# Kernel tuning notes

Measured on AMD Instinct MI355X. Metric: run time of the kernel, lower is better.

The kernel has to match this reference:

```python
import jax, jax.numpy as jnp
import numpy as np
from jax import lax

K = 16  # number of KNN neighbors (fixed in module)


def _knn_neighbors(x, k):
    # x: (B, 3, N) point coordinates -> neighbor coords (B, 3, N, K)
    inner = jnp.einsum('bdn,bdm->bnm', x, x)          # (B, N, N)
    sq = jnp.sum(x * x, axis=1)                        # (B, N)
    d2 = sq[:, :, None] + sq[:, None, :] - 2.0 * inner  # pairwise sq dists (B, N, N)
    _, nbr_idx = lax.top_k(-d2, k)                     # k nearest (incl. self), (B, N, K)
    # gather neighbor coordinates: expand x to (B, 3, 1, N), idx to (B, 1, N, K)
    neighbor = jnp.take_along_axis(x[:, :, None, :], nbr_idx[:, None, :, :], axis=3)
    return neighbor  # (B, 3, N, K)


def _down_index(neighbor, x, npts_ds):
    # center-diff saliency: sum of squared offsets to K neighbors per point
    diff = neighbor - x[:, :, :, None]                 # (B, 3, N, K)
    score = jnp.sum(diff * diff, axis=(1, 3))          # (B, N)
    _, idx = lax.top_k(score, npts_ds)                 # (B, npts_ds)
    return idx


def setup_inputs() -> dict:
    key = jax.random.key(0)
    k1, k2 = jax.random.split(key)
    B, N, C = 8, 4096, 128
    x = jax.random.normal(k1, (B, 3, N), dtype=jnp.float32)
    y = jax.random.normal(k2, (B, C, N), dtype=jnp.float32)
    return {"x": x, "y": y, "npts_ds": 2048}


def reference(x, y, npts_ds):
    B, _, N = x.shape
    C = y.shape[1]
    neighbor = _knn_neighbors(x, K)                    # ops.group(x, K, 'neighbor')
    idx = _down_index(neighbor, x, npts_ds)            # ops.down_index(...), (B, npts_ds)
    idx3 = jnp.broadcast_to(idx[:, None, :], (B, 3, npts_ds))
    idxC = jnp.broadcast_to(idx[:, None, :], (B, C, npts_ds))
    top_k_xyz = jnp.take_along_axis(x, idx3, axis=2)    # (B, 3, npts_ds)
    top_k_points = jnp.take_along_axis(y, idxC, axis=2)  # (B, C, npts_ds)
    return (top_k_xyz, top_k_points)
```

## Files before the change

### kernel.cpp

```cpp
#include <hip/hip_runtime.h>
#include <math.h>

#define BATCH 8
#define NPTS 4096
#define CHAN 128
#define KNN 16
#define SPLIT 4
#define CHUNK (NPTS / SPLIT)
#define ISPLIT 2
#define QCH (CHUNK / ISPLIT)
#define PCAP 24
#define RSPLIT 4
#define RCHUNK (NPTS / RSPLIT)

typedef unsigned long long u64;

__device__ __forceinline__ u64 pack_key(float d2, int idx) {
  unsigned b = __float_as_uint(d2);
  b ^= (unsigned)((int)b >> 31) | 0x80000000u;
  return ((u64)b << 32) | (unsigned)idx;
}

__device__ __forceinline__ float d2_ref(float4 q, float ppx, float ppy,
                                        float ppz, float psq) {
  float inner = __fadd_rn(__fadd_rn(__fmul_rn(ppx, q.x), __fmul_rn(ppy, q.y)),
                          __fmul_rn(ppz, q.z));
  return __fsub_rn(__fadd_rn(psq, q.w), __fmul_rn(2.0f, inner));
}

__device__ __forceinline__ void ce_asc(u64& x, u64& y) {
  bool sw = y < x;
  u64 lo = sw ? y : x;
  u64 hi = sw ? x : y;
  x = lo;
  y = hi;
}

__device__ __forceinline__ void bitonic_sort32(u64 a[32]) {
#pragma unroll
  for (int k = 2; k <= 32; k <<= 1) {
#pragma unroll
    for (int j = k >> 1; j > 0; j >>= 1) {
#pragma unroll
      for (int i = 0; i < 32; ++i) {
        int l = i ^ j;
        if (l > i) {
          if ((i & k) == 0) ce_asc(a[i], a[l]);
          else              ce_asc(a[l], a[i]);
        }
      }
    }
  }
}

__device__ __forceinline__ void merge_keep16(u64 T[16], const u64 A[16]) {
  u64 nt[16];
#pragma unroll
  for (int i = 0; i < 16; ++i) {
    u64 a = A[15 - i];
    nt[i] = (a < T[i]) ? a : T[i];
  }
#pragma unroll
  for (int j = 8; j > 0; j >>= 1) {
#pragma unroll
    for (int i = 0; i < 16; ++i) {
      int l = i ^ j;
      if (l > i) ce_asc(nt[i], nt[l]);
    }
  }
#pragma unroll
  for (int i = 0; i < 16; ++i) T[i] = nt[i];
}

__device__ __forceinline__ void ce_i32(int& x, int& y) {
  int lo = (x < y) ? x : y;
  int hi = (x < y) ? y : x;
  x = lo;
  y = hi;
}

__device__ __forceinline__ void batcher_sort16_i32(int a[16]) {
#define CE(i, j) ce_i32(a[i], a[j])
  CE(0, 8); CE(1, 9); CE(2, 10); CE(3, 11);
  CE(4, 12); CE(5, 13); CE(6, 14); CE(7, 15);
  CE(0, 4); CE(1, 5); CE(2, 6); CE(3, 7);
  CE(8, 12); CE(9, 13); CE(10, 14); CE(11, 15);
  CE(4, 8); CE(5, 9); CE(6, 10); CE(7, 11);
  CE(0, 2); CE(1, 3); CE(4, 6); CE(5, 7);
  CE(8, 10); CE(9, 11); CE(12, 14); CE(13, 15);
  CE(2, 8); CE(3, 9); CE(6, 12); CE(7, 13);
  CE(2, 4); CE(3, 5); CE(6, 8); CE(7, 9); CE(10, 12); CE(11, 13);
  CE(0, 1); CE(2, 3); CE(4, 5); CE(6, 7);
  CE(8, 9); CE(10, 11); CE(12, 13); CE(14, 15);
  CE(1, 8); CE(3, 10); CE(5, 12); CE(7, 14);
  CE(1, 4); CE(3, 6); CE(5, 8); CE(7, 10); CE(9, 12); CE(11, 14);
  CE(1, 2); CE(3, 4); CE(5, 6); CE(7, 8); CE(9, 10); CE(11, 12); CE(13, 14);
#undef CE
}

__device__ __forceinline__ void merge_keep16_i32(int T[16], const int A[16]) {
  int nt[16];
#pragma unroll
  for (int i = 0; i < 16; ++i) {
    int a = A[15 - i];
    nt[i] = (a < T[i]) ? a : T[i];
  }
#pragma unroll
  for (int j = 8; j > 0; j >>= 1) {
#pragma unroll
    for (int i = 0; i < 16; ++i) {
      int l = i ^ j;
      if (l > i) ce_i32(nt[i], nt[l]);
    }
  }
#pragma unroll
  for (int i = 0; i < 16; ++i) T[i] = nt[i];
}

__global__ __attribute__((amdgpu_waves_per_eu(4, 4)))
__launch_bounds__(512) void knn_partial_kernel(
    const float* __restrict__ x, u64* __restrict__ pkey) {
  const int s = blockIdx.x % SPLIT;
  const int ntile = (blockIdx.x / SPLIT) % (NPTS / 256);
  const int b = blockIdx.x / (SPLIT * (NPTS / 256));
  const int p = threadIdx.x & 255;
  const int h = threadIdx.x >> 8;
  __shared__ float4 xs[CHUNK];
  __shared__ unsigned short idxbuf[512 * PCAP];
  __shared__ u64 mbuf[KNN][256];

  const float* xb = x + (size_t)b * 3 * NPTS;
  for (int i = threadIdx.x; i < CHUNK; i += 512) {
    int gm = s * CHUNK + i;
    float px = xb[gm];
    float py = xb[NPTS + gm];
    float pz = xb[2 * NPTS + gm];
    float sq = __fadd_rn(__fadd_rn(__fmul_rn(px, px), __fmul_rn(py, py)),
                         __fmul_rn(pz, pz));
    xs[i] = make_float4(px, py, pz, sq);
  }

  const int n = ntile * 256 + p;
  float ppx = xb[n];
  float ppy = xb[NPTS + n];
  float ppz = xb[2 * NPTS + n];
  float psq = __fadd_rn(__fadd_rn(__fmul_rn(ppx, ppx), __fmul_rn(ppy, ppy)),
                        __fmul_rn(ppz, ppz));
  __syncthreads();

  const int cbase = h * QCH;

  int T[16];
#pragma unroll
  for (int i = 0; i < 16; ++i) T[i] = 0x7FFFFFFF;

  for (int base = 0; base < QCH; base += 16) {
    int A[16];
#pragma unroll
    for (int t = 0; t < 16; ++t) {
      float4 q = xs[cbase + base + t];
      A[t] = __float_as_int(d2_ref(q, ppx, ppy, ppz, psq));
    }
    batcher_sort16_i32(A);
    merge_keep16_i32(T, A);
  }
  const int v15 = T[15];

  unsigned short* mybuf = &idxbuf[(unsigned)threadIdx.x * PCAP];
  int cnt = 0;
#pragma unroll 4
  for (int m = 0; m < QCH; ++m) {
    float4 q = xs[cbase + m];
    int bits = __float_as_int(d2_ref(q, ppx, ppy, ppz, psq));
    if (bits <= v15) {
      mybuf[cnt < PCAP - 1 ? cnt : PCAP - 1] = (unsigned short)(cbase + m);
      ++cnt;
    }
  }

  u64 K[32];
#pragma unroll
  for (int j = 0; j < PCAP; ++j) {
    int loc = mybuf[j] & (CHUNK - 1);
    float4 q = xs[loc];
    float d2 = d2_ref(q, ppx, ppy, ppz, psq);
    u64 k = pack_key(d2, s * CHUNK + loc);
    K[j] = (j < cnt) ? k : ~0ull;
  }
#pragma unroll
  for (int j = PCAP; j < 32; ++j) K[j] = ~0ull;
  bitonic_sort32(K);

  if (h == 1) {
#pragma unroll
    for (int j = 0; j < 16; ++j) mbuf[j][p] = K[j];
  }
  __syncthreads();
  if (h == 0) {
    u64 T64[16];
#pragma unroll
    for (int j = 0; j < 16; ++j) T64[j] = K[j];
    u64 A64[16];
#pragma unroll
    for (int j = 0; j < 16; ++j) A64[j] = mbuf[j][p];
    merge_keep16(T64, A64);
    u64* pb = pkey + ((size_t)(b * SPLIT + s) * KNN) * NPTS + n;
#pragma unroll
    for (int j = 0; j < 16; ++j) pb[(size_t)j * NPTS] = T64[j];
  }
}

__global__ __attribute__((amdgpu_waves_per_eu(1, 2)))
__launch_bounds__(256) void merge_score_kernel(
    const float* __restrict__ x, const u64* __restrict__ pkey,
    float* __restrict__ score, int* __restrict__ cnt) {
  const int b = blockIdx.x / (NPTS / 256);
  const int n = (blockIdx.x % (NPTS / 256)) * 256 + threadIdx.x;

  cnt[(size_t)b * NPTS + n] = 0;

  u64 T[16];
  {
    const u64* pb = pkey + ((size_t)(b * SPLIT + 0) * KNN) * NPTS + n;
#pragma unroll
    for (int j = 0; j < 16; ++j) T[j] = pb[(size_t)j * NPTS];
  }
#pragma unroll
  for (int s = 1; s < SPLIT; ++s) {
    const u64* pb = pkey + ((size_t)(b * SPLIT + s) * KNN) * NPTS + n;
    u64 A[16];
#pragma unroll
    for (int j = 0; j < 16; ++j) A[j] = pb[(size_t)j * NPTS];
    merge_keep16(T, A);
  }

  const float* xb = x + (size_t)b * 3 * NPTS;
  float ppx = xb[n];
  float ppy = xb[NPTS + n];
  float ppz = xb[2 * NPTS + n];

  float nx[KNN], ny[KNN], nz[KNN];
#pragma unroll
  for (int j = 0; j < KNN; ++j) {
    int idx = (int)(unsigned)T[j];
    nx[j] = xb[idx];
    ny[j] = xb[NPTS + idx];
    nz[j] = xb[2 * NPTS + idx];
  }

  float P[3];
#pragma unroll
  for (int d = 0; d < 3; ++d) {
    const float pc = (d == 0) ? ppx : ((d == 1) ? ppy : ppz);
    float r[8];
#pragma unroll
    for (int j = 0; j < 8; ++j) {
      float c0 = (d == 0) ? nx[j] : ((d == 1) ? ny[j] : nz[j]);
      float c1 = (d == 0) ? nx[j + 8] : ((d == 1) ? ny[j + 8] : nz[j + 8]);
      float e0 = __fsub_rn(c0, pc);
      float e1 = __fsub_rn(c1, pc);
      r[j] = __fadd_rn(__fmul_rn(e0, e0), __fmul_rn(e1, e1));
    }
    float t0 = __fadd_rn(r[0], r[1]);
    float t1 = __fadd_rn(r[2], r[3]);
    float t2 = __fadd_rn(r[4], r[5]);
    float t3 = __fadd_rn(r[6], r[7]);
    P[d] = __fadd_rn(__fadd_rn(t0, t1), __fadd_rn(t2, t3));
  }
  score[(size_t)b * NPTS + n] =
      __fadd_rn(__fadd_rn(P[0], P[1]), P[2]);
}

__global__ __launch_bounds__(256) void rank_partial_kernel(
    const float* __restrict__ score, int* __restrict__ cnt) {
  const int s = blockIdx.x % RSPLIT;
  const int ntile = (blockIdx.x / RSPLIT) % (NPTS / 256);
  const int b = blockIdx.x / (RSPLIT * (NPTS / 256));
  __shared__ float ss[RCHUNK];

  const float* sb = score + (size_t)b * NPTS;
  for (int i = threadIdx.x; i < RCHUNK; i += 256)
    ss[i] = sb[s * RCHUNK + i];

  const int n = ntile * 256 + threadIdx.x;
  const float sn = sb[n];
  __syncthreads();

  int c = 0;
#pragma unroll 8
  for (int mm = 0; mm < RCHUNK; ++mm) {
    float sm = ss[mm];
    int gm = s * RCHUNK + mm;
    c += (sm > sn) || (sm == sn && gm < n);
  }
  atomicAdd(&cnt[(size_t)b * NPTS + n], c);
}

__global__ __launch_bounds__(256) void rank_scatter_kernel(
    const int* __restrict__ cnt, int* __restrict__ sel, int npts) {
  int t = blockIdx.x * 256 + threadIdx.x;
  int b = t / NPTS;
  int n = t % NPTS;
  int c = cnt[t];
  if (c < npts) sel[(size_t)b * npts + c] = n;
}

__global__ __launch_bounds__(256) void gather_kernel(
    const float* __restrict__ x, const float* __restrict__ y,
    const int* __restrict__ sel, float* __restrict__ out, int npts,
    int total0, int total) {
  int tid = blockIdx.x * blockDim.x + threadIdx.x;
  if (tid >= total) return;
  if (tid < total0) {
    int j = tid % npts;
    int rest = tid / npts;
    int d = rest % 3;
    int b = rest / 3;
    int src = sel[b * npts + j];
    out[tid] = x[((size_t)b * 3 + d) * NPTS + src];
  } else {
    int t = tid - total0;
    int j = t % npts;
    int rest = t / npts;
    int c = rest % CHAN;
    int b = rest / CHAN;
    int src = sel[b * npts + j];
    out[tid] = y[((size_t)b * CHAN + c) * NPTS + src];
  }
}

extern "C" void kernel_launch(void* const* d_in, const int* in_sizes, int n_in,
                              void* d_out, int out_size, void* d_ws,
                              size_t ws_size, hipStream_t stream) {
  const float* x = (const float*)d_in[0];
  const float* y = (const float*)d_in[1];
  float* out = (float*)d_out;

  const int npts = out_size / (BATCH * (3 + CHAN));

  char* w = (char*)d_ws;
  u64* pkey = (u64*)w;
  w += sizeof(u64) * (size_t)BATCH * SPLIT * KNN * NPTS;
  float* score = (float*)w;
  w += sizeof(float) * (size_t)BATCH * NPTS;
  int* cnt = (int*)w;
  w += sizeof(int) * (size_t)BATCH * NPTS;
  int* sel = (int*)w;

  knn_partial_kernel<<<BATCH * (NPTS / 256) * SPLIT, 512, 0, stream>>>(
      x, pkey);
  merge_score_kernel<<<BATCH * NPTS / 256, 256, 0, stream>>>(x, pkey, score,
                                                             cnt);
  rank_partial_kernel<<<BATCH * (NPTS / 256) * RSPLIT, 256, 0, stream>>>(
      score, cnt);
  rank_scatter_kernel<<<BATCH * NPTS / 256, 256, 0, stream>>>(cnt, sel, npts);

  const int total0 = BATCH * 3 * npts;
  gather_kernel<<<(out_size + 255) / 256, 256, 0, stream>>>(
      x, y, sel, out, npts, total0, out_size);
}
```

Measured before the change: 268.3 us.

## Embed candidate index in truncated distance bits to skip rescan pass

Packs the local candidate index into the low 9 mantissa bits of each int-cast distance, so the running top-16 carries indices directly. A 17th-smallest tracker detects ties at the truncated threshold. Only in that case does it fall back to the full rescan-and-collect pass. The common path instead recomputes exact distances for the 16 kept candidates and sorts them with a 16-element network, removing a full second sweep over the chunk and the 32-element bitonic sort. The cost is extra min/max work per batch to maintain the 17th value, plus thread divergence when some lanes take the slow path.

```diff
diff --git a/kernel.cpp b/kernel.cpp
--- a/kernel.cpp
+++ b/kernel.cpp
@@ -9,7 +9,7 @@
 #define CHUNK (NPTS / SPLIT)
 #define ISPLIT 2
 #define QCH (CHUNK / ISPLIT)
-#define PCAP 24
+#define EPC 24
 #define RSPLIT 4
 #define RCHUNK (NPTS / RSPLIT)
 
@@ -34,6 +34,25 @@
   u64 hi = sw ? x : y;
   x = lo;
   y = hi;
+}
+
+__device__ __forceinline__ void batcher_sort16_u64(u64 a[16]) {
+#define CE(i, j) ce_asc(a[i], a[j])
+  CE(0, 8); CE(1, 9); CE(2, 10); CE(3, 11);
+  CE(4, 12); CE(5, 13); CE(6, 14); CE(7, 15);
+  CE(0, 4); CE(1, 5); CE(2, 6); CE(3, 7);
+  CE(8, 12); CE(9, 13); CE(10, 14); CE(11, 15);
+  CE(4, 8); CE(5, 9); CE(6, 10); CE(7, 11);
+  CE(0, 2); CE(1, 3); CE(4, 6); CE(5, 7);
+  CE(8, 10); CE(9, 11); CE(12, 14); CE(13, 15);
+  CE(2, 8); CE(3, 9); CE(6, 12); CE(7, 13);
+  CE(2, 4); CE(3, 5); CE(6, 8); CE(7, 9); CE(10, 12); CE(11, 13);
+  CE(0, 1); CE(2, 3); CE(4, 5); CE(6, 7);
+  CE(8, 9); CE(10, 11); CE(12, 13); CE(14, 15);
+  CE(1, 8); CE(3, 10); CE(5, 12); CE(7, 14);
+  CE(1, 4); CE(3, 6); CE(5, 8); CE(7, 10); CE(9, 12); CE(11, 14);
+  CE(1, 2); CE(3, 4); CE(5, 6); CE(7, 8); CE(9, 10); CE(11, 12); CE(13, 14);
+#undef CE
 }
 
 __device__ __forceinline__ void bitonic_sort32(u64 a[32]) {
@@ -126,7 +145,7 @@
   const int p = threadIdx.x & 255;
   const int h = threadIdx.x >> 8;
   __shared__ float4 xs[CHUNK];
-  __shared__ unsigned short idxbuf[512 * PCAP];
+  __shared__ unsigned short ebuf[512 * EPC];
   __shared__ u64 mbuf[KNN][256];
 
   const float* xb = x + (size_t)b * 3 * NPTS;
@@ -153,43 +172,75 @@
   int T[16];
 #pragma unroll
   for (int i = 0; i < 16; ++i) T[i] = 0x7FFFFFFF;
-
+  int r17 = 0x7FFFFFFF;
+
+#pragma unroll 1
   for (int base = 0; base < QCH; base += 16) {
     int A[16];
 #pragma unroll
     for (int t = 0; t < 16; ++t) {
       float4 q = xs[cbase + base + t];
-      A[t] = __float_as_int(d2_ref(q, ppx, ppy, ppz, psq));
+      int bits = __float_as_int(d2_ref(q, ppx, ppy, ppz, psq));
+      A[t] = (bits & 0xFFFFFE00) | (base + t);
     }
     batcher_sort16_i32(A);
+    int u[16];
+#pragma unroll
+    for (int i = 0; i < 16; ++i) {
+      int a = A[15 - i];
+      u[i] = (T[i] < a) ? a : T[i];
+    }
+#pragma unroll
+    for (int w = 8; w > 0; w >>= 1) {
+#pragma unroll
+      for (int i = 0; i < 16; ++i) {
+        if (i < w) u[i] = (u[i] < u[i + w]) ? u[i] : u[i + w];
+      }
+    }
+    r17 = (r17 < u[0]) ? r17 : u[0];
     merge_keep16_i32(T, A);
   }
-  const int v15 = T[15];
-
-  unsigned short* mybuf = &idxbuf[(unsigned)threadIdx.x * PCAP];
-  int cnt = 0;
+
+  const int tau = T[15] & 0xFFFFFE00;
+  const bool slow = ((r17 & 0xFFFFFE00) == tau);
+
+  u64 K[16];
+  if (!slow) {
+#pragma unroll
+    for (int j = 0; j < 16; ++j) {
+      int loc = cbase + (T[j] & 511);
+      float4 q = xs[loc];
+      float d2 = d2_ref(q, ppx, ppy, ppz, psq);
+      K[j] = pack_key(d2, s * CHUNK + loc);
+    }
+    batcher_sort16_u64(K);
+  } else {
+    unsigned short* myb = &ebuf[(unsigned)threadIdx.x * EPC];
+    int cnt = 0;
 #pragma unroll 4
-  for (int m = 0; m < QCH; ++m) {
-    float4 q = xs[cbase + m];
-    int bits = __float_as_int(d2_ref(q, ppx, ppy, ppz, psq));
-    if (bits <= v15) {
-      mybuf[cnt < PCAP - 1 ? cnt : PCAP - 1] = (unsigned short)(cbase + m);
-      ++cnt;
-    }
-  }
-
-  u64 K[32];
-#pragma unroll
-  for (int j = 0; j < PCAP; ++j) {
-    int loc = mybuf[j] & (CHUNK - 1);
-    float4 q = xs[loc];
-    float d2 = d2_ref(q, ppx, ppy, ppz, psq);
-    u64 k = pack_key(d2, s * CHUNK + loc);
-    K[j] = (j < cnt) ? k : ~0ull;
-  }
-#pragma unroll
-  for (int j = PCAP; j < 32; ++j) K[j] = ~0ull;
-  bitonic_sort32(K);
+    for (int m = 0; m < QCH; ++m) {
+      float4 q = xs[cbase + m];
+      int tb = __float_as_int(d2_ref(q, ppx, ppy, ppz, psq)) & 0xFFFFFE00;
+      if (tb <= tau) {
+        myb[cnt < EPC - 1 ? cnt : EPC - 1] = (unsigned short)m;
+        ++cnt;
+      }
+    }
+    u64 KK[32];
+#pragma unroll
+    for (int j = 0; j < EPC; ++j) {
+      int loc = cbase + (myb[j] & 511);
+      float4 q = xs[loc];
+      float d2 = d2_ref(q, ppx, ppy, ppz, psq);
+      u64 k = pack_key(d2, s * CHUNK + loc);
+      KK[j] = (j < cnt) ? k : ~0ull;
+    }
+#pragma unroll
+    for (int j = EPC; j < 32; ++j) KK[j] = ~0ull;
+    bitonic_sort32(KK);
+#pragma unroll
+    for (int j = 0; j < 16; ++j) K[j] = KK[j];
+  }
 
   if (h == 1) {
 #pragma unroll
@@ -197,16 +248,13 @@
   }
   __syncthreads();
   if (h == 0) {
-    u64 T64[16];
-#pragma unroll
-    for (int j = 0; j < 16; ++j) T64[j] = K[j];
     u64 A64[16];
 #pragma unroll
     for (int j = 0; j < 16; ++j) A64[j] = mbuf[j][p];
-    merge_keep16(T64, A64);
+    merge_keep16(K, A64);
     u64* pb = pkey + ((size_t)(b * SPLIT + s) * KNN) * NPTS + n;
 #pragma unroll
-    for (int j = 0; j < 16; ++j) pb[(size_t)j * NPTS] = T64[j];
+    for (int j = 0; j < 16; ++j) pb[(size_t)j * NPTS] = K[j];
   }
 }
 
```

Measured after the change: 256.0 us. 1.05x faster.
